# Kernel tuning notes

Hardware: AMD Instinct MI355X
Metric: run time of the kernel (lower is better)

## Reference

```python
import jax, jax.numpy as jnp
import numpy as np

S, N, IN = 4096, 32, 4
H, IF, SF, OUT = 64, 8, 4, 2
N_PAIRS = N * (N - 1)


def setup_inputs() -> dict:
    key = jax.random.key(0)
    ks = jax.random.split(key, 12)
    f = jax.random.normal
    return {
        "inputs": f(ks[0], (S, N, IN), jnp.float32),
        "L1W": f(ks[1], (H, IN), jnp.float32) * 0.1,
        "L1b": f(ks[2], (H,), jnp.float32) * 0.1,
        "L2W": f(ks[3], (H, H), jnp.float32) * 0.1,
        "L2b": f(ks[4], (H,), jnp.float32) * 0.1,
        "I1W": f(ks[5], (H, H), jnp.float32) * 0.1,
        "I2W": f(ks[6], (IF, H), jnp.float32) * 0.1,
        "I3": f(ks[7], (N_PAIRS, OUT, IF // OUT), jnp.float32) * 0.01,
        "S1W": f(ks[8], (SF, IN), jnp.float32) * 0.1,
        "S1b": f(ks[9], (SF,), jnp.float32) * 0.1,
        "S2W": f(ks[10], (N, OUT, SF // OUT), jnp.float32) * 0.01,
        "S2b": jnp.zeros((N, OUT), jnp.float32),
    }


def reference(inputs, L1W, L1b, L2W, L2b, I1W, I2W, I3, S1W, S1b, S2W, S2b):
    seq_len, n_obj = inputs.shape[:2]
    out_size = S2b.shape[1]

    # shared encoders (torch Linear: x @ W.T + b)
    h = jax.nn.relu(inputs @ L1W.T + L1b)
    h = jax.nn.relu(h @ L2W.T + L2b)          # [S, N, H]
    hs = jax.nn.relu(inputs @ S1W.T + S1b)    # [S, N, SF]

    # all pairwise differences Xi - Xj -> edge MLP (no biases)
    diff = h[:, :, None, :] - h[:, None, :, :]      # [S, N, N, H]
    pair = jnp.tanh(diff @ I1W.T)                   # [S, N, N, H]
    pair = jnp.tanh(pair @ I2W.T)                   # [S, N, N, IF]
    k_int = pair.shape[-1] // out_size
    pair = pair.reshape(seq_len, n_obj, n_obj, out_size, k_int)

    # scatter per-pair weights I3 into dense [N, N, OUT, k] using the
    # row-major Table ordering (i, j != i); diagonal stays zero, which
    # matches the original since diag pairwise features are exactly 0.
    ii, jj = np.nonzero(~np.eye(n_obj, dtype=bool))
    I3d = jnp.zeros((n_obj, n_obj, out_size, k_int), I3.dtype).at[ii, jj].set(I3)

    interaction = jnp.einsum('sijdk,ijdk->sid', pair, I3d)  # [S, N, OUT]

    k_self = hs.shape[-1] // out_size
    hs = hs.reshape(seq_len, n_obj, out_size, k_self)
    self_term = jnp.einsum('sidk,idk->sid', hs, S2W) + S2b  # [S, N, OUT]

    return interaction + self_term
```

## Files before the change

### kernel.cpp

```cpp
#include <hip/hip_runtime.h>
#include <math.h>

#define SEQ   4096
#define NOBJ  32
#define IN_F  4
#define HID   64
#define IFEAT 8
#define NPAIR_HALF 496
#define NTILE 31

#define TWO_LOG2E 2.8853900817779268f
#define GP_CLAMP  10.0f

#if __has_builtin(__builtin_amdgcn_exp2f)
  #define EXP2F(x) __builtin_amdgcn_exp2f(x)
#else
  #define EXP2F(x) exp2f(x)
#endif

#if __has_builtin(__builtin_amdgcn_rcph)
  #define RCPH(x) __builtin_amdgcn_rcph(x)
#else
  #define RCPH(x) ((_Float16)__builtin_amdgcn_rcpf((float)(x)))
#endif

typedef _Float16 h2    __attribute__((ext_vector_type(2)));
typedef _Float16 f16x8 __attribute__((ext_vector_type(8)));
typedef float    f32x4 __attribute__((ext_vector_type(4)));

__device__ __forceinline__ h2 pack2(float a, float b) {
  return __builtin_bit_cast(h2, __builtin_amdgcn_cvt_pkrtz(a, b));
}
__device__ __forceinline__ unsigned pbits(h2 v) { return __builtin_bit_cast(unsigned, v); }

__device__ __forceinline__ f16x8 pack8(float4 a, float4 b) {
  int4 v;
  v.x = (int)pbits(pack2(a.x, a.y));
  v.y = (int)pbits(pack2(a.z, a.w));
  v.z = (int)pbits(pack2(b.x, b.y));
  v.w = (int)pbits(pack2(b.z, b.w));
  return __builtin_bit_cast(f16x8, v);
}

__device__ __forceinline__ float tanh_u(float x) {
  float e = EXP2F(x * TWO_LOG2E);
  float r = __builtin_amdgcn_rcpf(e + 1.0f);
  return fmaf(-2.0f, r, 1.0f);
}

__device__ __forceinline__ int pair_cum(int i) { return (i * (63 - i)) >> 1; }

__device__ __forceinline__ void pair_decode(int q, int& i, int& j) {
  int ii = (int)((63.0f - sqrtf(3969.0f - 8.0f * (float)q)) * 0.5f);
  if (ii > 0 && pair_cum(ii) > q) --ii;
  if (pair_cum(ii + 1) <= q)     ++ii;
  i = ii;
  j = ii + 1 + (q - pair_cum(ii));
}

__global__ __launch_bounds__(256, 4) void magnet_fused(
    const float* __restrict__ x,
    const float* __restrict__ L1W,
    const float* __restrict__ L1b,
    const float* __restrict__ L2W,
    const float* __restrict__ L2b,
    const float* __restrict__ I1W,
    const float* __restrict__ I2W,
    const float* __restrict__ I3,
    const float* __restrict__ S1W,
    const float* __restrict__ S1b,
    const float* __restrict__ S2W,
    const float* __restrict__ S2b,
    float* __restrict__ out)
{
  __shared__ __align__(16) float smem[8424];
  unsigned*       sEd0 = (unsigned*)(smem + 2304);
  unsigned*       wB   = (unsigned*)(smem + 6592);
  float*          part = smem + 6592;
  float*          sx   = smem + 7104;
  float*          sW   = smem + 7360;
  unsigned*       ptab32 = (unsigned*)(smem + 7368);
  unsigned short* ptab2  = (unsigned short*)(smem + 7864);
  float*          swpart = smem + 8360;

  const int t  = threadIdx.x;
  const int s0 = blockIdx.x * 2;

  sx[t] = x[s0 * 128 + t];
  if (t < 64) {
    const int f = t >> 3, seg = t & 7;
    const float4 a = *(const float4*)(I2W + f * HID + seg * 8);
    const float4 b = *(const float4*)(I2W + f * HID + seg * 8 + 4);
    swpart[t] = ((a.x + a.y) + (a.z + a.w)) + ((b.x + b.y) + (b.z + b.w));
  }
  #pragma unroll
  for (int idx = t; idx < 512; idx += 256) {
    const int n = idx >> 5, k2 = idx & 31;
    wB[idx] = (n < IFEAT)
      ? pbits(pack2(I2W[n * HID + 2 * k2], I2W[n * HID + 2 * k2 + 1])) : 0u;
  }
  #pragma unroll
  for (int q = t; q < NPAIR_HALF; q += 256) {
    int i, j; pair_decode(q, i, j);
    ptab32[q] = ((unsigned)(i * 36) << 16) | (unsigned)(j * 36);
  }
  #pragma unroll
  for (int idx = t; idx < 992; idx += 256) {
    const int i = (idx * 2115) >> 16;
    const int m = idx - i * 31;
    const int j = m + (m >= i);
    unsigned v;
    if (j > i) v = (unsigned)(pair_cum(i) + (j - i - 1));
    else       v = (unsigned)(pair_cum(j) + (i - j - 1)) | 0x8000u;
    ptab2[idx] = (unsigned short)v;
  }
  __syncthreads();
  if (t < IFEAT) {
    float a = 0.0f;
    #pragma unroll
    for (int c = 0; c < 8; ++c) a += swpart[t * 8 + c];
    sW[t] = a;
  }

  {
    const int n = t & 31, gI = t >> 5, kb = gI * 8;
    float a[2][8];
    #pragma unroll
    for (int r = 0; r < 8; ++r) {
      const int k = kb + r;
      const float4 w = *(const float4*)(L1W + k * 4);
      const float bias = L1b[k];
      #pragma unroll
      for (int ss = 0; ss < 2; ++ss) {
        const float* xv = sx + ss * 128 + n * 4;
        float v = bias;
        v = fmaf(xv[0], w.x, v); v = fmaf(xv[1], w.y, v);
        v = fmaf(xv[2], w.z, v); v = fmaf(xv[3], w.w, v);
        a[ss][r] = fmaxf(v, 0.0f);
      }
    }
    #pragma unroll
    for (int ss = 0; ss < 2; ++ss) {
      unsigned* sAtp = (unsigned*)(smem + ss * 1152);
      int4 pk;
      pk.x = (int)pbits(pack2(a[ss][0], a[ss][1]));
      pk.y = (int)pbits(pack2(a[ss][2], a[ss][3]));
      pk.z = (int)pbits(pack2(a[ss][4], a[ss][5]));
      pk.w = (int)pbits(pack2(a[ss][6], a[ss][7]));
      *(int4*)(sAtp + n * 36 + gI * 4) = pk;
    }
  }
  __syncthreads();

  const int lane = t & 63;
  const int wv   = t >> 6;
  const int qd   = lane >> 4;
  const int ln   = lane & 15;

  {
    const int m = 16 * wv + ln;
    const float* wr = L2W + m * HID;
    const f16x8 A0 = pack8(*(const float4*)(wr + 8 * qd),
                           *(const float4*)(wr + 8 * qd + 4));
    const f16x8 A1 = pack8(*(const float4*)(wr + 32 + 8 * qd),
                           *(const float4*)(wr + 32 + 8 * qd + 4));
    const float4 bias = *(const float4*)(L2b + 16 * wv + 4 * qd);
    unsigned pk[2][4];
    #pragma unroll
    for (int ss = 0; ss < 2; ++ss) {
      const unsigned* sAtp = (const unsigned*)(smem + ss * 1152);
      #pragma unroll
      for (int nt = 0; nt < 2; ++nt) {
        const int n = nt * 16 + ln;
        const f16x8 B0 = __builtin_bit_cast(f16x8, *(const int4*)(sAtp + n * 36 + 4 * qd));
        const f16x8 B1 = __builtin_bit_cast(f16x8, *(const int4*)(sAtp + n * 36 + 16 + 4 * qd));
        f32x4 c; c[0] = bias.x; c[1] = bias.y; c[2] = bias.z; c[3] = bias.w;
        c = __builtin_amdgcn_mfma_f32_16x16x32_f16(A0, B0, c, 0, 0, 0);
        c = __builtin_amdgcn_mfma_f32_16x16x32_f16(A1, B1, c, 0, 0, 0);
        pk[ss][nt * 2]     = pbits(pack2(fmaxf(c[0], 0.f), fmaxf(c[1], 0.f)));
        pk[ss][nt * 2 + 1] = pbits(pack2(fmaxf(c[2], 0.f), fmaxf(c[3], 0.f)));
      }
    }
    __syncthreads();
    #pragma unroll
    for (int ss = 0; ss < 2; ++ss) {
      unsigned* sBtp = (unsigned*)(smem + ss * 1152);
      #pragma unroll
      for (int nt = 0; nt < 2; ++nt) {
        const int n = nt * 16 + ln;
        sBtp[n * 36 + 8 * wv + 2 * qd]     = pk[ss][nt * 2];
        sBtp[n * 36 + 8 * wv + 2 * qd + 1] = pk[ss][nt * 2 + 1];
      }
    }
  }
  __syncthreads();

  {
    const int m = 16 * wv + ln;
    const float* wr = I1W + m * HID;
    const f16x8 A0 = pack8(*(const float4*)(wr + 8 * qd),
                           *(const float4*)(wr + 8 * qd + 4));
    const f16x8 A1 = pack8(*(const float4*)(wr + 32 + 8 * qd),
                           *(const float4*)(wr + 32 + 8 * qd + 4));
    #pragma unroll
    for (int ss = 0; ss < 2; ++ss) {
      const unsigned* sBtp = (const unsigned*)(smem + ss * 1152);
      unsigned* sEd = sEd0 + ss * 1152;
      #pragma unroll
      for (int nt = 0; nt < 2; ++nt) {
        const int n = nt * 16 + ln;
        const f16x8 B0 = __builtin_bit_cast(f16x8, *(const int4*)(sBtp + n * 36 + 4 * qd));
        const f16x8 B1 = __builtin_bit_cast(f16x8, *(const int4*)(sBtp + n * 36 + 16 + 4 * qd));
        f32x4 c; c[0] = 0.f; c[1] = 0.f; c[2] = 0.f; c[3] = 0.f;
        c = __builtin_amdgcn_mfma_f32_16x16x32_f16(A0, B0, c, 0, 0, 0);
        c = __builtin_amdgcn_mfma_f32_16x16x32_f16(A1, B1, c, 0, 0, 0);
        float e[4];
        #pragma unroll
        for (int r = 0; r < 4; ++r) {
          float gp = fminf(fmaxf(c[r] * TWO_LOG2E, -GP_CLAMP), GP_CLAMP);
          e[r] = EXP2F(gp);
        }
        sEd[n * 36 + 8 * wv + 2 * qd]     = pbits(pack2(e[0], e[1]));
        sEd[n * 36 + 8 * wv + 2 * qd + 1] = pbits(pack2(e[2], e[3]));
      }
    }
  }
  __syncthreads();

  {
    const f16x8 B0 = __builtin_bit_cast(f16x8, *(const int4*)(wB + ln * 32 + 4 * qd));
    const f16x8 B1 = __builtin_bit_cast(f16x8, *(const int4*)(wB + ln * 32 + 16 + 4 * qd));
    const float Wf = sW[ln & 7];

    for (int tile = wv; tile < NTILE; tile += 4) {
      const unsigned pij = ptab32[tile * 16 + ln];
      const int io = (int)(pij >> 16), jo = (int)(pij & 0xffffu);
      #pragma unroll
      for (int ss = 0; ss < 2; ++ss) {
        const unsigned* sEd = sEd0 + ss * 1152;
        _Float16* sv = ss ? (_Float16*)(smem + 4608) : (_Float16*)smem;
        const f16x8 ei0 = __builtin_bit_cast(f16x8, *(const int4*)(sEd + io + 4 * qd));
        const f16x8 ei1 = __builtin_bit_cast(f16x8, *(const int4*)(sEd + io + 16 + 4 * qd));
        const f16x8 fj0 = __builtin_bit_cast(f16x8, *(const int4*)(sEd + jo + 4 * qd));
        const f16x8 fj1 = __builtin_bit_cast(f16x8, *(const int4*)(sEd + jo + 16 + 4 * qd));
        const f16x8 su0 = ei0 + fj0;
        const f16x8 su1 = ei1 + fj1;
        f16x8 q0, q1;
        #pragma unroll
        for (int k = 0; k < 8; ++k) { q0[k] = RCPH(su0[k]); q1[k] = RCPH(su1[k]); }
        const f16x8 A0 = fj0 * q0;
        const f16x8 A1 = fj1 * q1;
        f32x4 c; c[0] = 0.f; c[1] = 0.f; c[2] = 0.f; c[3] = 0.f;
        c = __builtin_amdgcn_mfma_f32_16x16x32_f16(A0, B0, c, 0, 0, 0);
        c = __builtin_amdgcn_mfma_f32_16x16x32_f16(A1, B1, c, 0, 0, 0);
        if (ln < IFEAT) {
          #pragma unroll
          for (int r = 0; r < 4; ++r) {
            const float v = tanh_u(fmaf(-2.0f, c[r], Wf));
            sv[(tile * 16 + 4 * qd + r) * 8 + ln] = (_Float16)v;
          }
        }
      }
    }
  }
  __syncthreads();

  {
    const int ss = t >> 7, i = (t >> 2) & 31, d = (t >> 1) & 1, half = t & 1;
    const _Float16* sv = ss ? (const _Float16*)(smem + 4608) : (const _Float16*)smem;
    const int msta = half * 16;
    const int mend = half ? 31 : 16;
    float sum = 0.0f;
    for (int m = msta; m < mend; ++m) {
      const unsigned pv = ptab2[i * 31 + m];
      const int q = (int)(pv & 0x7fffu);
      const h2* vp = (const h2*)(sv + q * 8 + d * 4);
      const h2 va = vp[0], vb = vp[1];
      const float4 cf = *(const float4*)(I3 + (i * 31 + m) * 8 + d * 4);
      float dot;
      dot = cf.x * (float)va.x;
      dot = fmaf(cf.y, (float)va.y, dot);
      dot = fmaf(cf.z, (float)vb.x, dot);
      dot = fmaf(cf.w, (float)vb.y, dot);
      sum += (pv & 0x8000u) ? -dot : dot;
    }
    part[t] = sum;
  }
  __syncthreads();

  if (t < 128) {
    const int ss = t >> 6, i = (t >> 1) & 31, d = t & 1;
    const int pbase = ss * 128 + i * 4 + d * 2;
    float sum = part[pbase] + part[pbase + 1];

    float res = S2b[i * 2 + d] + sum;
    const float* xv = sx + ss * 128 + i * 4;
    #pragma unroll
    for (int k = 0; k < 2; ++k) {
      const int f = d * 2 + k;
      float hs = S1b[f];
      hs = fmaf(xv[0], S1W[f * 4 + 0], hs);
      hs = fmaf(xv[1], S1W[f * 4 + 1], hs);
      hs = fmaf(xv[2], S1W[f * 4 + 2], hs);
      hs = fmaf(xv[3], S1W[f * 4 + 3], hs);
      hs = fmaxf(hs, 0.0f);
      res = fmaf(hs, S2W[i * 4 + d * 2 + k], res);
    }
    out[(s0 + ss) * (NOBJ * 2) + i * 2 + d] = res;
  }
}

extern "C" void kernel_launch(void* const* d_in, const int* in_sizes, int n_in,
                              void* d_out, int out_size, void* d_ws, size_t ws_size,
                              hipStream_t stream) {
  const float* x   = (const float*)d_in[0];
  const float* L1W = (const float*)d_in[1];
  const float* L1b = (const float*)d_in[2];
  const float* L2W = (const float*)d_in[3];
  const float* L2b = (const float*)d_in[4];
  const float* I1W = (const float*)d_in[5];
  const float* I2W = (const float*)d_in[6];
  const float* I3  = (const float*)d_in[7];
  const float* S1W = (const float*)d_in[8];
  const float* S1b = (const float*)d_in[9];
  const float* S2W = (const float*)d_in[10];
  const float* S2b = (const float*)d_in[11];
  float* outp = (float*)d_out;

  magnet_fused<<<SEQ / 2, 256, 0, stream>>>(x, L1W, L1b, L2W, L2b, I1W, I2W, I3,
                                            S1W, S1b, S2W, S2b, outp);
}
```

Measured before the change: 114.7 us.

## Double block size so each half of the threads handles one sequence step

The block grows from 256 to 512 threads, and each 256-thread half processes one of the two sequence steps. This replaces the per-thread loops over both steps in the encoder, edge-MLP and pair stages. The final interaction reduction is split four ways instead of two, and table setup loops collapse to single iterations. The aim is more waves in flight per block to hide latency. In exchange, the launch bound of (512, 8) may squeeze the register budget and cause spills, and each block now needs more resources at once.

```diff
diff --git a/kernel.cpp b/kernel.cpp
--- a/kernel.cpp
+++ b/kernel.cpp
@@ -58,7 +58,7 @@
   j = ii + 1 + (q - pair_cum(ii));
 }
 
-__global__ __launch_bounds__(256, 4) void magnet_fused(
+__global__ __launch_bounds__(512, 8) void magnet_fused(
     const float* __restrict__ x,
     const float* __restrict__ L1W,
     const float* __restrict__ L1b,
@@ -86,26 +86,24 @@
   const int t  = threadIdx.x;
   const int s0 = blockIdx.x * 2;
 
-  sx[t] = x[s0 * 128 + t];
+  if (t < 256) sx[t] = x[s0 * 128 + t];
   if (t < 64) {
     const int f = t >> 3, seg = t & 7;
     const float4 a = *(const float4*)(I2W + f * HID + seg * 8);
     const float4 b = *(const float4*)(I2W + f * HID + seg * 8 + 4);
     swpart[t] = ((a.x + a.y) + (a.z + a.w)) + ((b.x + b.y) + (b.z + b.w));
   }
+  {
+    const int n = t >> 5, k2 = t & 31;
+    wB[t] = (n < IFEAT)
+      ? pbits(pack2(I2W[n * HID + 2 * k2], I2W[n * HID + 2 * k2 + 1])) : 0u;
+  }
+  if (t < NPAIR_HALF) {
+    int i, j; pair_decode(t, i, j);
+    ptab32[t] = ((unsigned)(i * 36) << 16) | (unsigned)(j * 36);
+  }
   #pragma unroll
-  for (int idx = t; idx < 512; idx += 256) {
-    const int n = idx >> 5, k2 = idx & 31;
-    wB[idx] = (n < IFEAT)
-      ? pbits(pack2(I2W[n * HID + 2 * k2], I2W[n * HID + 2 * k2 + 1])) : 0u;
-  }
-  #pragma unroll
-  for (int q = t; q < NPAIR_HALF; q += 256) {
-    int i, j; pair_decode(q, i, j);
-    ptab32[q] = ((unsigned)(i * 36) << 16) | (unsigned)(j * 36);
-  }
-  #pragma unroll
-  for (int idx = t; idx < 992; idx += 256) {
+  for (int idx = t; idx < 992; idx += 512) {
     const int i = (idx * 2115) >> 16;
     const int m = idx - i * 31;
     const int j = m + (m >= i);
@@ -123,106 +121,92 @@
   }
 
   {
-    const int n = t & 31, gI = t >> 5, kb = gI * 8;
-    float a[2][8];
+    const int n = t & 31, gI = (t >> 5) & 7, ssp = t >> 8, kb = gI * 8;
+    const float* xv = sx + ssp * 128 + n * 4;
+    float a[8];
     #pragma unroll
     for (int r = 0; r < 8; ++r) {
       const int k = kb + r;
       const float4 w = *(const float4*)(L1W + k * 4);
-      const float bias = L1b[k];
-      #pragma unroll
-      for (int ss = 0; ss < 2; ++ss) {
-        const float* xv = sx + ss * 128 + n * 4;
-        float v = bias;
-        v = fmaf(xv[0], w.x, v); v = fmaf(xv[1], w.y, v);
-        v = fmaf(xv[2], w.z, v); v = fmaf(xv[3], w.w, v);
-        a[ss][r] = fmaxf(v, 0.0f);
-      }
-    }
-    #pragma unroll
-    for (int ss = 0; ss < 2; ++ss) {
-      unsigned* sAtp = (unsigned*)(smem + ss * 1152);
-      int4 pk;
-      pk.x = (int)pbits(pack2(a[ss][0], a[ss][1]));
-      pk.y = (int)pbits(pack2(a[ss][2], a[ss][3]));
-      pk.z = (int)pbits(pack2(a[ss][4], a[ss][5]));
-      pk.w = (int)pbits(pack2(a[ss][6], a[ss][7]));
-      *(int4*)(sAtp + n * 36 + gI * 4) = pk;
-    }
+      float v = L1b[k];
+      v = fmaf(xv[0], w.x, v); v = fmaf(xv[1], w.y, v);
+      v = fmaf(xv[2], w.z, v); v = fmaf(xv[3], w.w, v);
+      a[r] = fmaxf(v, 0.0f);
+    }
+    unsigned* sAtp = (unsigned*)(smem + ssp * 1152);
+    int4 pk;
+    pk.x = (int)pbits(pack2(a[0], a[1]));
+    pk.y = (int)pbits(pack2(a[2], a[3]));
+    pk.z = (int)pbits(pack2(a[4], a[5]));
+    pk.w = (int)pbits(pack2(a[6], a[7]));
+    *(int4*)(sAtp + n * 36 + gI * 4) = pk;
   }
   __syncthreads();
 
   const int lane = t & 63;
   const int wv   = t >> 6;
+  const int wq   = wv & 3;
+  const int ssw  = wv >> 2;
   const int qd   = lane >> 4;
   const int ln   = lane & 15;
 
   {
-    const int m = 16 * wv + ln;
+    const int m = 16 * wq + ln;
     const float* wr = L2W + m * HID;
     const f16x8 A0 = pack8(*(const float4*)(wr + 8 * qd),
                            *(const float4*)(wr + 8 * qd + 4));
     const f16x8 A1 = pack8(*(const float4*)(wr + 32 + 8 * qd),
                            *(const float4*)(wr + 32 + 8 * qd + 4));
-    const float4 bias = *(const float4*)(L2b + 16 * wv + 4 * qd);
-    unsigned pk[2][4];
-    #pragma unroll
-    for (int ss = 0; ss < 2; ++ss) {
-      const unsigned* sAtp = (const unsigned*)(smem + ss * 1152);
-      #pragma unroll
-      for (int nt = 0; nt < 2; ++nt) {
-        const int n = nt * 16 + ln;
-        const f16x8 B0 = __builtin_bit_cast(f16x8, *(const int4*)(sAtp + n * 36 + 4 * qd));
-        const f16x8 B1 = __builtin_bit_cast(f16x8, *(const int4*)(sAtp + n * 36 + 16 + 4 * qd));
-        f32x4 c; c[0] = bias.x; c[1] = bias.y; c[2] = bias.z; c[3] = bias.w;
-        c = __builtin_amdgcn_mfma_f32_16x16x32_f16(A0, B0, c, 0, 0, 0);
-        c = __builtin_amdgcn_mfma_f32_16x16x32_f16(A1, B1, c, 0, 0, 0);
-        pk[ss][nt * 2]     = pbits(pack2(fmaxf(c[0], 0.f), fmaxf(c[1], 0.f)));
-        pk[ss][nt * 2 + 1] = pbits(pack2(fmaxf(c[2], 0.f), fmaxf(c[3], 0.f)));
-      }
+    const float4 bias = *(const float4*)(L2b + 16 * wq + 4 * qd);
+    unsigned pk[4];
+    const unsigned* sAtp = (const unsigned*)(smem + ssw * 1152);
+    #pragma unroll
+    for (int nt = 0; nt < 2; ++nt) {
+      const int n = nt * 16 + ln;
+      const f16x8 B0 = __builtin_bit_cast(f16x8, *(const int4*)(sAtp + n * 36 + 4 * qd));
+      const f16x8 B1 = __builtin_bit_cast(f16x8, *(const int4*)(sAtp + n * 36 + 16 + 4 * qd));
+      f32x4 c; c[0] = bias.x; c[1] = bias.y; c[2] = bias.z; c[3] = bias.w;
+      c = __builtin_amdgcn_mfma_f32_16x16x32_f16(A0, B0, c, 0, 0, 0);
+      c = __builtin_amdgcn_mfma_f32_16x16x32_f16(A1, B1, c, 0, 0, 0);
+      pk[nt * 2]     = pbits(pack2(fmaxf(c[0], 0.f), fmaxf(c[1], 0.f)));
+      pk[nt * 2 + 1] = pbits(pack2(fmaxf(c[2], 0.f), fmaxf(c[3], 0.f)));
     }
     __syncthreads();
-    #pragma unroll
-    for (int ss = 0; ss < 2; ++ss) {
-      unsigned* sBtp = (unsigned*)(smem + ss * 1152);
-      #pragma unroll
-      for (int nt = 0; nt < 2; ++nt) {
-        const int n = nt * 16 + ln;
-        sBtp[n * 36 + 8 * wv + 2 * qd]     = pk[ss][nt * 2];
-        sBtp[n * 36 + 8 * wv + 2 * qd + 1] = pk[ss][nt * 2 + 1];
-      }
-    }
-  }
-  __syncthreads();
-
-  {
-    const int m = 16 * wv + ln;
+    unsigned* sBtp = (unsigned*)(smem + ssw * 1152);
+    #pragma unroll
+    for (int nt = 0; nt < 2; ++nt) {
+      const int n = nt * 16 + ln;
+      sBtp[n * 36 + 8 * wq + 2 * qd]     = pk[nt * 2];
+      sBtp[n * 36 + 8 * wq + 2 * qd + 1] = pk[nt * 2 + 1];
+    }
+  }
+  __syncthreads();
+
+  {
+    const int m = 16 * wq + ln;
     const float* wr = I1W + m * HID;
     const f16x8 A0 = pack8(*(const float4*)(wr + 8 * qd),
                            *(const float4*)(wr + 8 * qd + 4));
     const f16x8 A1 = pack8(*(const float4*)(wr + 32 + 8 * qd),
                            *(const float4*)(wr + 32 + 8 * qd + 4));
-    #pragma unroll
-    for (int ss = 0; ss < 2; ++ss) {
-      const unsigned* sBtp = (const unsigned*)(smem + ss * 1152);
-      unsigned* sEd = sEd0 + ss * 1152;
+    const unsigned* sBtp = (const unsigned*)(smem + ssw * 1152);
+    unsigned* sEd = sEd0 + ssw * 1152;
+    #pragma unroll
+    for (int nt = 0; nt < 2; ++nt) {
+      const int n = nt * 16 + ln;
+      const f16x8 B0 = __builtin_bit_cast(f16x8, *(const int4*)(sBtp + n * 36 + 4 * qd));
+      const f16x8 B1 = __builtin_bit_cast(f16x8, *(const int4*)(sBtp + n * 36 + 16 + 4 * qd));
+      f32x4 c; c[0] = 0.f; c[1] = 0.f; c[2] = 0.f; c[3] = 0.f;
+      c = __builtin_amdgcn_mfma_f32_16x16x32_f16(A0, B0, c, 0, 0, 0);
+      c = __builtin_amdgcn_mfma_f32_16x16x32_f16(A1, B1, c, 0, 0, 0);
+      float e[4];
       #pragma unroll
-      for (int nt = 0; nt < 2; ++nt) {
-        const int n = nt * 16 + ln;
-        const f16x8 B0 = __builtin_bit_cast(f16x8, *(const int4*)(sBtp + n * 36 + 4 * qd));
-        const f16x8 B1 = __builtin_bit_cast(f16x8, *(const int4*)(sBtp + n * 36 + 16 + 4 * qd));
-        f32x4 c; c[0] = 0.f; c[1] = 0.f; c[2] = 0.f; c[3] = 0.f;
-        c = __builtin_amdgcn_mfma_f32_16x16x32_f16(A0, B0, c, 0, 0, 0);
-        c = __builtin_amdgcn_mfma_f32_16x16x32_f16(A1, B1, c, 0, 0, 0);
-        float e[4];
-        #pragma unroll
-        for (int r = 0; r < 4; ++r) {
-          float gp = fminf(fmaxf(c[r] * TWO_LOG2E, -GP_CLAMP), GP_CLAMP);
-          e[r] = EXP2F(gp);
-        }
-        sEd[n * 36 + 8 * wv + 2 * qd]     = pbits(pack2(e[0], e[1]));
-        sEd[n * 36 + 8 * wv + 2 * qd + 1] = pbits(pack2(e[2], e[3]));
+      for (int r = 0; r < 4; ++r) {
+        float gp = fminf(fmaxf(c[r] * TWO_LOG2E, -GP_CLAMP), GP_CLAMP);
+        e[r] = EXP2F(gp);
       }
+      sEd[n * 36 + 8 * wq + 2 * qd]     = pbits(pack2(e[0], e[1]));
+      sEd[n * 36 + 8 * wq + 2 * qd + 1] = pbits(pack2(e[2], e[3]));
     }
   }
   __syncthreads();
@@ -231,34 +215,31 @@
     const f16x8 B0 = __builtin_bit_cast(f16x8, *(const int4*)(wB + ln * 32 + 4 * qd));
     const f16x8 B1 = __builtin_bit_cast(f16x8, *(const int4*)(wB + ln * 32 + 16 + 4 * qd));
     const float Wf = sW[ln & 7];
-
-    for (int tile = wv; tile < NTILE; tile += 4) {
+    const unsigned* sEd = sEd0 + ssw * 1152;
+    _Float16* sv = ssw ? (_Float16*)(smem + 4608) : (_Float16*)smem;
+
+    for (int tile = wq; tile < NTILE; tile += 4) {
       const unsigned pij = ptab32[tile * 16 + ln];
       const int io = (int)(pij >> 16), jo = (int)(pij & 0xffffu);
+      const f16x8 ei0 = __builtin_bit_cast(f16x8, *(const int4*)(sEd + io + 4 * qd));
+      const f16x8 ei1 = __builtin_bit_cast(f16x8, *(const int4*)(sEd + io + 16 + 4 * qd));
+      const f16x8 fj0 = __builtin_bit_cast(f16x8, *(const int4*)(sEd + jo + 4 * qd));
+      const f16x8 fj1 = __builtin_bit_cast(f16x8, *(const int4*)(sEd + jo + 16 + 4 * qd));
+      const f16x8 su0 = ei0 + fj0;
+      const f16x8 su1 = ei1 + fj1;
+      f16x8 q0, q1;
       #pragma unroll
-      for (int ss = 0; ss < 2; ++ss) {
-        const unsigned* sEd = sEd0 + ss * 1152;
-        _Float16* sv = ss ? (_Float16*)(smem + 4608) : (_Float16*)smem;
-        const f16x8 ei0 = __builtin_bit_cast(f16x8, *(const int4*)(sEd + io + 4 * qd));
-        const f16x8 ei1 = __builtin_bit_cast(f16x8, *(const int4*)(sEd + io + 16 + 4 * qd));
-        const f16x8 fj0 = __builtin_bit_cast(f16x8, *(const int4*)(sEd + jo + 4 * qd));
-        const f16x8 fj1 = __builtin_bit_cast(f16x8, *(const int4*)(sEd + jo + 16 + 4 * qd));
-        const f16x8 su0 = ei0 + fj0;
-        const f16x8 su1 = ei1 + fj1;
-        f16x8 q0, q1;
+      for (int k = 0; k < 8; ++k) { q0[k] = RCPH(su0[k]); q1[k] = RCPH(su1[k]); }
+      const f16x8 A0 = fj0 * q0;
+      const f16x8 A1 = fj1 * q1;
+      f32x4 c; c[0] = 0.f; c[1] = 0.f; c[2] = 0.f; c[3] = 0.f;
+      c = __builtin_amdgcn_mfma_f32_16x16x32_f16(A0, B0, c, 0, 0, 0);
+      c = __builtin_amdgcn_mfma_f32_16x16x32_f16(A1, B1, c, 0, 0, 0);
+      if (ln < IFEAT) {
         #pragma unroll
-        for (int k = 0; k < 8; ++k) { q0[k] = RCPH(su0[k]); q1[k] = RCPH(su1[k]); }
-        const f16x8 A0 = fj0 * q0;
-        const f16x8 A1 = fj1 * q1;
-        f32x4 c; c[0] = 0.f; c[1] = 0.f; c[2] = 0.f; c[3] = 0.f;
-        c = __builtin_amdgcn_mfma_f32_16x16x32_f16(A0, B0, c, 0, 0, 0);
-        c = __builtin_amdgcn_mfma_f32_16x16x32_f16(A1, B1, c, 0, 0, 0);
-        if (ln < IFEAT) {
-          #pragma unroll
-          for (int r = 0; r < 4; ++r) {
-            const float v = tanh_u(fmaf(-2.0f, c[r], Wf));
-            sv[(tile * 16 + 4 * qd + r) * 8 + ln] = (_Float16)v;
-          }
+        for (int r = 0; r < 4; ++r) {
+          const float v = tanh_u(fmaf(-2.0f, c[r], Wf));
+          sv[(tile * 16 + 4 * qd + r) * 8 + ln] = (_Float16)v;
         }
       }
     }
@@ -266,10 +247,10 @@
   __syncthreads();
 
   {
-    const int ss = t >> 7, i = (t >> 2) & 31, d = (t >> 1) & 1, half = t & 1;
-    const _Float16* sv = ss ? (const _Float16*)(smem + 4608) : (const _Float16*)smem;
-    const int msta = half * 16;
-    const int mend = half ? 31 : 16;
+    const int ssp = t >> 8, i = (t >> 3) & 31, d = (t >> 2) & 1, mq = t & 3;
+    const _Float16* sv = ssp ? (const _Float16*)(smem + 4608) : (const _Float16*)smem;
+    const int msta = mq * 8;
+    const int mend = (mq == 3) ? 31 : (msta + 8);
     float sum = 0.0f;
     for (int m = msta; m < mend; ++m) {
       const unsigned pv = ptab2[i * 31 + m];
@@ -289,12 +270,12 @@
   __syncthreads();
 
   if (t < 128) {
-    const int ss = t >> 6, i = (t >> 1) & 31, d = t & 1;
-    const int pbase = ss * 128 + i * 4 + d * 2;
-    float sum = part[pbase] + part[pbase + 1];
+    const int ssp = t >> 6, i = (t >> 1) & 31, d = t & 1;
+    const int pbase = ssp * 256 + i * 8 + d * 4;
+    float sum = (part[pbase] + part[pbase + 1]) + (part[pbase + 2] + part[pbase + 3]);
 
     float res = S2b[i * 2 + d] + sum;
-    const float* xv = sx + ss * 128 + i * 4;
+    const float* xv = sx + ssp * 128 + i * 4;
     #pragma unroll
     for (int k = 0; k < 2; ++k) {
       const int f = d * 2 + k;
@@ -306,7 +287,7 @@
       hs = fmaxf(hs, 0.0f);
       res = fmaf(hs, S2W[i * 4 + d * 2 + k], res);
     }
-    out[(s0 + ss) * (NOBJ * 2) + i * 2 + d] = res;
+    out[(s0 + ssp) * (NOBJ * 2) + i * 2 + d] = res;
   }
 }
 
@@ -327,6 +308,6 @@
   const float* S2b = (const float*)d_in[11];
   float* outp = (float*)d_out;
 
-  magnet_fused<<<SEQ / 2, 256, 0, stream>>>(x, L1W, L1b, L2W, L2b, I1W, I2W, I3,
+  magnet_fused<<<SEQ / 2, 512, 0, stream>>>(x, L1W, L1b, L2W, L2b, I1W, I2W, I3,
                                             S1W, S1b, S2W, S2b, outp);
 }
```

New measurement: 119.4 us. 1.04x slower.
